# Performance work log

Measured on AMD Instinct MI355X. Metric: run time of the kernel, lower is better.

Reference implementation:

```python
import jax, jax.numpy as jnp
import numpy as np


def setup_inputs() -> dict:
    key = jax.random.key(0)
    k1, k2, k3 = jax.random.split(key, 3)
    B, D, H = 16384, 256, 64
    X = jax.random.normal(k1, (B, D), dtype=jnp.float32)
    AUX = jax.random.normal(k2, (B, (1 + D) * H), dtype=jnp.float32)
    K = jax.random.randint(k3, (B,), 0, 129, dtype=jnp.int64)  # idx in [0, M=128]
    return {"X": X, "AUX": AUX, "K": K}


def reference(X, AUX, K):
    B, D = X.shape
    H = AUX.shape[1] // (1 + D)
    M = D // 2
    # Per-sample weight matrix W[b] of shape (1+D, H)
    W = AUX.reshape(B, 1 + D, H)
    # Original zeros rows idx:M and M+idx: (end), i.e. keeps row j iff
    #   j < idx  OR  (M <= j < M + idx)
    j = jnp.arange(1 + D)  # row indices 0..D (row D is the bias row)
    Kc = K[:, None]
    keep = (j < Kc) | ((j >= M) & (j < M + Kc))  # [B, 1+D] bool
    # Y[b] = concat(X[b], 1.0); apply mask to Y instead of W (same dot product)
    Y = jnp.concatenate([X, jnp.ones((B, 1), dtype=X.dtype)], axis=1)
    Ym = Y * keep.astype(X.dtype)
    dot = jnp.einsum("bj,bjh->bh", Ym, W)  # [B, H]
    return jnp.tanh(dot)
```

## Files before the change

### kernel.cpp

```cpp
#include <hip/hip_runtime.h>
#include <cmath>


#define D_DIM 256
#define H_DIM 64
#define ROWS 257
#define ROWSTRIDE (ROWS * H_DIM)

typedef float vf4 __attribute__((ext_vector_type(4)));

__device__ __forceinline__ vf4 ldnt(const float* p)
{
    return __builtin_nontemporal_load(reinterpret_cast<const vf4*>(p));
}

__global__ __launch_bounds__(256, 8)
void dotmask_kernel(const float* __restrict__ X,
                    const float* __restrict__ AUX,
                    const int* __restrict__ K,
                    float* __restrict__ out)
{
    const int b    = blockIdx.x;
    const int tid  = threadIdx.x;
    const int lane = tid & 63;
    const int w    = tid >> 6;
    const int jo   = lane >> 4;
    const int h4   = (lane & 15) * 4;

    const int k = K[b];
    const float* __restrict__ Wb  = AUX + (size_t)b * ROWSTRIDE;
    const float* __restrict__ WbH = Wb + h4;
    const float* __restrict__ Xb  = X   + (size_t)b * D_DIM;

    __shared__ float xm[ROWS + 3];
    {
        const bool keep = (tid < k) | ((tid >= 128) & (tid < 128 + k));
        float xv = 0.f;
        if (keep) xv = Xb[tid];
        xm[tid] = xv;
        if (tid == 0) xm[256] = 0.f;
    }
    __syncthreads();

    float ax = 0.f, ay = 0.f, az = 0.f, aw = 0.f;

    const int C  = (k + 3) >> 2;
    const int lo = (C * w) >> 2;
    const int hi = (C * (w + 1)) >> 2;

    for (int c = lo; c < hi; c += 2) {
        const int ja = 4 * c + jo;
        if (ja < k) {
            const vf4 wa1 = ldnt(WbH + ((size_t)ja         << 6));
            const vf4 wa2 = ldnt(WbH + ((size_t)(ja + 128) << 6));
            const float xa1 = xm[ja];
            const float xa2 = xm[ja + 128];
            ax += xa1 * wa1[0]; ay += xa1 * wa1[1]; az += xa1 * wa1[2]; aw += xa1 * wa1[3];
            ax += xa2 * wa2[0]; ay += xa2 * wa2[1]; az += xa2 * wa2[2]; aw += xa2 * wa2[3];
        }

        if (c + 1 < hi) {
            const int jb = 4 * (c + 1) + jo;
            if (jb < k) {
                const vf4 wb1 = ldnt(WbH + ((size_t)jb         << 6));
                const vf4 wb2 = ldnt(WbH + ((size_t)(jb + 128) << 6));
                const float xb1 = xm[jb];
                const float xb2 = xm[jb + 128];
                ax += xb1 * wb1[0]; ay += xb1 * wb1[1]; az += xb1 * wb1[2]; aw += xb1 * wb1[3];
                ax += xb2 * wb2[0]; ay += xb2 * wb2[1]; az += xb2 * wb2[2]; aw += xb2 * wb2[3];
            }
        }
    }

    if (k > 128 && w == 0 && jo == 0) {
        const vf4 wv = ldnt(Wb + (size_t)256 * H_DIM + h4);
        ax += wv[0]; ay += wv[1]; az += wv[2]; aw += wv[3];
    }

    ax += __shfl_xor(ax, 16); ay += __shfl_xor(ay, 16);
    az += __shfl_xor(az, 16); aw += __shfl_xor(aw, 16);
    ax += __shfl_xor(ax, 32); ay += __shfl_xor(ay, 32);
    az += __shfl_xor(az, 32); aw += __shfl_xor(aw, 32);

    __shared__ float red[4][H_DIM];
    if (lane < 16) {
        float4 p; p.x = ax; p.y = ay; p.z = az; p.w = aw;
        *reinterpret_cast<float4*>(&red[w][h4]) = p;
    }
    __syncthreads();

    if (tid < H_DIM) {
        const float s = red[0][tid] + red[1][tid] + red[2][tid] + red[3][tid];
        __builtin_nontemporal_store(tanhf(s), out + (size_t)b * H_DIM + tid);
    }
}

extern "C" void kernel_launch(void* const* d_in, const int* in_sizes, int n_in,
                              void* d_out, int out_size, void* d_ws, size_t ws_size,
                              hipStream_t stream)
{
    const float* X   = (const float*)d_in[0];
    const float* AUX = (const float*)d_in[1];
    const int*   K   = (const int*)d_in[2];
    float* out = (float*)d_out;

    const int B = in_sizes[2];
    dotmask_kernel<<<B, 256, 0, stream>>>(X, AUX, K, out);
}
```

Baseline: 98.49 us.

## Schedule blocks in descending K order via counting sort for load balance

```diff
diff --git a/kernel.cpp b/kernel.cpp
--- a/kernel.cpp
+++ b/kernel.cpp
@@ -7,6 +7,10 @@
 #define ROWS 257
 #define ROWSTRIDE (ROWS * H_DIM)
 
+#define WS_COUNTS 0
+#define WS_CURSOR 256
+#define WS_ORDER  512
+
 typedef float vf4 __attribute__((ext_vector_type(4)));
 
 __device__ __forceinline__ vf4 ldnt(const float* p)
@@ -14,13 +18,46 @@
     return __builtin_nontemporal_load(reinterpret_cast<const vf4*>(p));
 }
 
+__global__ void count_kernel(const int* __restrict__ K, int* __restrict__ counts, int B)
+{
+    const int i = blockIdx.x * 256 + threadIdx.x;
+    if (i < B) atomicAdd(&counts[K[i]], 1);
+}
+
+__global__ void scan_kernel(const int* __restrict__ counts, int* __restrict__ cursor)
+{
+    __shared__ int s[256];
+    const int t = threadIdx.x;
+    const int v = (t < 129) ? counts[128 - t] : 0;
+    s[t] = v;
+    __syncthreads();
+    for (int off = 1; off < 256; off <<= 1) {
+        const int x = (t >= off) ? s[t - off] : 0;
+        __syncthreads();
+        s[t] += x;
+        __syncthreads();
+    }
+    if (t < 129) cursor[128 - t] = s[t] - v;
+}
+
+__global__ void scatter_kernel(const int* __restrict__ K, int* __restrict__ cursor,
+                               int* __restrict__ order, int B)
+{
+    const int i = blockIdx.x * 256 + threadIdx.x;
+    if (i < B) {
+        const int p = atomicAdd(&cursor[K[i]], 1);
+        order[p] = i;
+    }
+}
+
 __global__ __launch_bounds__(256, 8)
 void dotmask_kernel(const float* __restrict__ X,
                     const float* __restrict__ AUX,
                     const int* __restrict__ K,
+                    const int* __restrict__ order,
                     float* __restrict__ out)
 {
-    const int b    = blockIdx.x;
+    const int b    = order[blockIdx.x];
     const int tid  = threadIdx.x;
     const int lane = tid & 63;
     const int w    = tid >> 6;
@@ -103,7 +140,15 @@
     const float* AUX = (const float*)d_in[1];
     const int*   K   = (const int*)d_in[2];
     float* out = (float*)d_out;
+    int*   wsi = (int*)d_ws;
 
-    const int B = in_sizes[2];
-    dotmask_kernel<<<B, 256, 0, stream>>>(X, AUX, K, out);
+    const int B  = in_sizes[2];
+    const int nb = (B + 255) / 256;
+
+    hipMemsetAsync(wsi + WS_COUNTS, 0, 129 * sizeof(int), stream);
+    count_kernel  <<<nb, 256, 0, stream>>>(K, wsi + WS_COUNTS, B);
+    scan_kernel   <<<1, 256, 0, stream>>>(wsi + WS_COUNTS, wsi + WS_CURSOR);
+    scatter_kernel<<<nb, 256, 0, stream>>>(K, wsi + WS_CURSOR, wsi + WS_ORDER, B);
+
+    dotmask_kernel<<<B, 256, 0, stream>>>(X, AUX, K, wsi + WS_ORDER, out);
 }
```

Result: slower. 129.3 us (+31.3%).
